# Kernel tuning notes

Measured on AMD Instinct MI355X. Metric: run time of the kernel, lower is better.

Reference implementation:

```python
import jax, jax.numpy as jnp
import numpy as np

B, S, D = 4, 2048, 2048
E = 64           # num_experts
TOPK = 2         # num_experts_per_token


def setup_inputs() -> dict:
    key = jax.random.key(0)
    k1, k2, k3 = jax.random.split(key, 3)
    x_real = jax.random.normal(k1, (B, S, D), dtype=jnp.float32)
    x_imag = jax.random.normal(k2, (B, S, D), dtype=jnp.float32)
    # flax Dense: kernel [in_features, out_features] with lecun_normal-ish scale
    W = jax.random.normal(k3, (2 * D, E), dtype=jnp.float32) / np.sqrt(2.0 * D)
    b = jnp.zeros((E,), dtype=jnp.float32)
    return {"x_real": x_real, "x_imag": x_imag, "W": W, "b": b}


def reference(x_real, x_imag, W, b):
    # amp = |x|, phase = angle(x) for x = x_real + i*x_imag
    amp = jnp.hypot(x_real, x_imag)                 # [B,S,D]
    phase = jnp.arctan2(x_imag, x_real)             # [B,S,D]
    routing_input = jnp.concatenate([amp, phase], axis=-1)  # [B,S,2D]
    scores = jnp.einsum('bsf,fe->bse', routing_input, W) + b  # [B,S,E]
    probs = jax.nn.softmax(scores, axis=-1)
    top_k_probs, top_k_indices = jax.lax.top_k(probs, TOPK)   # [B,S,K]
    top_k_probs = top_k_probs / jnp.sum(top_k_probs, axis=-1, keepdims=True)
    return (top_k_probs, top_k_indices)
```

## Files before the change

### kernel.cpp

```cpp
#include <hip/hip_runtime.h>
#include <math.h>

#define NTOK 8192
#define DD   2048
#define EE   64
#define TSTRIP 16
#define NCH 16
#define PROB_N (NTOK*2)
#define AROW 136
#define F_PSTRIDE (128*4*64*8)

typedef _Float16 f16x8 __attribute__((ext_vector_type(8)));
typedef _Float16 f16x4 __attribute__((ext_vector_type(4)));
typedef float    f32x4 __attribute__((ext_vector_type(4)));

__device__ __forceinline__ f16x8 gload_f16x8(const _Float16* p) {
    f16x8 r;
    asm volatile("global_load_dwordx4 %0, %1, off" : "=v"(r) : "v"(p));
    return r;
}
__device__ __forceinline__ f32x4 gload_f32x4(const float* p) {
    f32x4 r;
    asm volatile("global_load_dwordx4 %0, %1, off" : "=v"(r) : "v"(p));
    return r;
}
#define VMWAIT(n) do { \
    asm volatile("s_waitcnt vmcnt(" #n ")" ::: "memory"); \
    __builtin_amdgcn_sched_barrier(0); \
} while (0)
#define LBAR() do { \
    asm volatile("s_waitcnt lgkmcnt(0)" ::: "memory"); \
    __builtin_amdgcn_s_barrier(); \
    __builtin_amdgcn_sched_barrier(0); \
} while (0)

__device__ __forceinline__ float fast_atan2f(float y, float x) {
    const float ax = __builtin_fabsf(x), ay = __builtin_fabsf(y);
    const float hi = fmaxf(ax, ay), lo = fminf(ax, ay);
    const bool  big = lo > 0.4142135679721832f * hi;
    const float num = big ? (lo - hi) : lo;
    const float den = big ? (lo + hi) : hi;
    float rc = __builtin_amdgcn_rcpf(den);
    rc = rc * fmaf(-den, rc, 2.0f);
    const float z  = num * rc;
    const float z2 = z * z;
    float p = fmaf(z2, 8.05374449538e-2f, -1.38776856032e-1f);
    p = fmaf(z2, p, 1.99777106478e-1f);
    p = fmaf(z2, p, -3.33329491539e-1f);
    float r = fmaf(z * z2, p, z);
    r = r + (big ? 0.78539816339744830962f : 0.0f);
    r = (ay > ax) ? (1.57079632679489661923f - r) : r;
    r = (x < 0.0f) ? (3.14159265358979323846f - r) : r;
    return copysignf(r, y);
}

__device__ __forceinline__ void fsplit2(float x, _Float16& h1, _Float16& h2s) {
    const _Float16 a = (_Float16)x;
    h1 = a;
    h2s = (_Float16)((x - (float)a) * 2048.0f);
}

__global__ __launch_bounds__(256) void wsplit(const float* __restrict__ W,
                                              _Float16* __restrict__ F) {
    const int g  = blockIdx.x * 256 + threadIdx.x;
    const int e  = g & 63;
    const int q  = g >> 6;
    const int d0 = q * 4;
    const int nt = e >> 4;
    const int lane = ((d0 & 31) >> 3) * 16 + (e & 15);
    const int j0 = d0 & 7;
    const int cka = 2 * (d0 >> 5);

    f16x4 a1, a2, p1, p2;
    #pragma unroll
    for (int i = 0; i < 4; ++i) {
        _Float16 h, l;
        fsplit2(W[(size_t)(d0 + i) * EE + e], h, l);      a1[i] = h; a2[i] = l;
        fsplit2(W[(size_t)(DD + d0 + i) * EE + e], h, l); p1[i] = h; p2[i] = l;
    }
    *(f16x4*)&F[((size_t)(0 * 128 + cka)     * 4 + nt) * 512 + lane * 8 + j0] = a1;
    *(f16x4*)&F[((size_t)(1 * 128 + cka)     * 4 + nt) * 512 + lane * 8 + j0] = a2;
    *(f16x4*)&F[((size_t)(0 * 128 + cka + 1) * 4 + nt) * 512 + lane * 8 + j0] = p1;
    *(f16x4*)&F[((size_t)(1 * 128 + cka + 1) * 4 + nt) * 512 + lane * 8 + j0] = p2;
}

__global__ __launch_bounds__(512, 4) void gemm_topk(
    const float* __restrict__ xr, const float* __restrict__ xi,
    const _Float16* __restrict__ F, const float* __restrict__ bias,
    float* __restrict__ out)
{
    __shared__ __align__(16) _Float16 A[2][2][2][TSTRIP][AROW];
    __shared__ float scoreH[2][TSTRIP][EE];

    const int tid = threadIdx.x;
    const int t0  = blockIdx.x * TSTRIP;
    const int wv = tid >> 6, lane = tid & 63;
    const int nt = wv & 3, kh = wv >> 2;
    const int fm = lane & 15, fq = lane >> 4;
    const int kh_s  = tid >> 8;
    const int tok_s = (tid >> 4) & 15;
    const int f4    = tid & 15;

    const float bv = bias[lane];

    const float* prx = xr + (size_t)(t0 + tok_s) * DD + kh_s * 1024 + f4 * 4;
    const float* pix = xi + (size_t)(t0 + tok_s) * DD + kh_s * 1024 + f4 * 4;
    const int posa = 64 * (f4 >> 3) + (f4 & 7) * 4;

    auto sprocess = [&](f32x4 vr, f32x4 vi, int buf) {
        f16x4 a1, a2, p1, p2;
        #pragma unroll
        for (int i = 0; i < 4; ++i) {
            const float amp = __builtin_amdgcn_sqrtf(fmaf(vr[i], vr[i], vi[i] * vi[i]));
            const float ph  = fast_atan2f(vi[i], vr[i]);
            _Float16 h, l;
            fsplit2(amp, h, l); a1[i] = h; a2[i] = l;
            fsplit2(ph,  h, l); p1[i] = h; p2[i] = l;
        }
        *(f16x4*)&A[buf][kh_s][0][tok_s][posa]      = a1;
        *(f16x4*)&A[buf][kh_s][1][tok_s][posa]      = a2;
        *(f16x4*)&A[buf][kh_s][0][tok_s][posa + 32] = p1;
        *(f16x4*)&A[buf][kh_s][1][tok_s][posa + 32] = p2;
    };

    f32x4 accH = (f32x4){0.f, 0.f, 0.f, 0.f};
    f32x4 accL = (f32x4){0.f, 0.f, 0.f, 0.f};

    const _Float16* bbase = F + ((size_t)(kh * 64) * 4 + nt) * 512 + lane * 8;

    f16x8 bh[2][4], bl[2][4];
    f32x4 xrb[2], xib[2];

    xrb[0] = gload_f32x4(prx);
    xib[0] = gload_f32x4(pix);
    #pragma unroll
    for (int j = 0; j < 4; ++j) {
        bh[0][j] = gload_f16x8(bbase + j * 2048);
        bl[0][j] = gload_f16x8(bbase + F_PSTRIDE + j * 2048);
    }
    VMWAIT(8);
    sprocess(xrb[0], xib[0], 0);
    xrb[1] = gload_f32x4(prx + 64);
    xib[1] = gload_f32x4(pix + 64);
    #pragma unroll
    for (int j = 0; j < 4; ++j) {
        bh[1][j] = gload_f16x8(bbase + 8192 + j * 2048);
        bl[1][j] = gload_f16x8(bbase + 8192 + F_PSTRIDE + j * 2048);
    }
    LBAR();

    #pragma unroll
    for (int c = 0; c < NCH; ++c) {
        const int buf = c & 1;
        if (c < NCH - 1) { VMWAIT(10); } else { VMWAIT(0); }
        #pragma unroll
        for (int j = 0; j < 4; ++j) {
            const f16x8 a1 = *(const f16x8*)&A[buf][kh][0][fm][j * 32 + fq * 8];
            const f16x8 a2 = *(const f16x8*)&A[buf][kh][1][fm][j * 32 + fq * 8];
            accH = __builtin_amdgcn_mfma_f32_16x16x32_f16(a1, bh[buf][j], accH, 0, 0, 0);
            accL = __builtin_amdgcn_mfma_f32_16x16x32_f16(a1, bl[buf][j], accL, 0, 0, 0);
            accL = __builtin_amdgcn_mfma_f32_16x16x32_f16(a2, bh[buf][j], accL, 0, 0, 0);
        }
        if (c < NCH - 1) {
            VMWAIT(8);
            sprocess(xrb[buf ^ 1], xib[buf ^ 1], buf ^ 1);
            if (c < NCH - 2) {
                xrb[buf] = gload_f32x4(prx + (c + 2) * 64);
                xib[buf] = gload_f32x4(pix + (c + 2) * 64);
                const _Float16* nb = bbase + (size_t)(c + 2) * 8192;
                #pragma unroll
                for (int j = 0; j < 4; ++j) {
                    bh[buf][j] = gload_f16x8(nb + j * 2048);
                    bl[buf][j] = gload_f16x8(nb + F_PSTRIDE + j * 2048);
                }
            }
            LBAR();
        }
    }

    #pragma unroll
    for (int r = 0; r < 4; ++r)
        scoreH[kh][fq * 4 + r][nt * 16 + fm] = fmaf(accL[r], 4.8828125e-4f, accH[r]);
    __syncthreads();

    #pragma unroll
    for (int rep = 0; rep < 2; ++rep) {
        const int tok = wv * 2 + rep;
        float v1 = scoreH[0][tok][lane] + scoreH[1][tok][lane] + bv;
        float v2 = -INFINITY;
        int   i1 = lane, i2 = 64;
        #pragma unroll
        for (int off = 1; off < 64; off <<= 1) {
            const float ov1 = __shfl_xor(v1, off, 64);
            const int   oi1 = __shfl_xor(i1, off, 64);
            const float ov2 = __shfl_xor(v2, off, 64);
            const int   oi2 = __shfl_xor(i2, off, 64);
            const bool b1 = (ov1 > v1) || (ov1 == v1 && oi1 < i1);
            const float n1 = b1 ? ov1 : v1;  const int ni1 = b1 ? oi1 : i1;
            const float c1 = b1 ? v1  : ov1; const int ci1 = b1 ? i1  : oi1;
            const float c2 = b1 ? ov2 : v2;  const int ci2 = b1 ? oi2 : i2;
            const bool b2 = (c1 > c2) || (c1 == c2 && ci1 < ci2);
            v1 = n1; i1 = ni1;
            v2 = b2 ? c1 : c2; i2 = b2 ? ci1 : ci2;
        }
        if (lane == 0) {
            const int t = t0 + tok;
            const float z  = expf(v2 - v1);
            const float p1 = 1.0f / (1.0f + z);
            const float p2 = z / (1.0f + z);
            out[(size_t)t * 2 + 0] = p1;
            out[(size_t)t * 2 + 1] = p2;
            out[PROB_N + (size_t)t * 2 + 0] = (float)i1;
            out[PROB_N + (size_t)t * 2 + 1] = (float)i2;
        }
    }
}

extern "C" void kernel_launch(void* const* d_in, const int* in_sizes, int n_in,
                              void* d_out, int out_size, void* d_ws, size_t ws_size,
                              hipStream_t stream) {
    const float* xr = (const float*)d_in[0];
    const float* xi = (const float*)d_in[1];
    const float* W  = (const float*)d_in[2];
    const float* b  = (const float*)d_in[3];
    float* out = (float*)d_out;
    _Float16* F = (_Float16*)d_ws;

    wsplit<<<128, 256, 0, stream>>>(W, F);
    gemm_topk<<<NTOK / TSTRIP, 512, 0, stream>>>(xr, xi, F, b, out);
}
```

Baseline: 172.5 us.

## Warp-specialize gemm_topk into producer and MFMA waves with LDS flag handshakes

Splits each 768-thread block into 8 MFMA consumer waves and 4 producer waves. The producers load x and compute amp and phase into a 3-slot LDS ring, and the two sides sync through per-chunk ready and done counters instead of block barriers. The token strip doubles to 32 so each consumer wave issues two MFMA row tiles per B fragment, which halves how often B is loaded from global memory per token. The aim is to overlap the heavy atan2 work with the matrix math. The cost is spin-wait polling, fewer blocks, and more LDS per block.

```diff
diff --git a/kernel.cpp b/kernel.cpp
--- a/kernel.cpp
+++ b/kernel.cpp
@@ -4,8 +4,9 @@
 #define NTOK 8192
 #define DD   2048
 #define EE   64
-#define TSTRIP 16
+#define TSTRIP 32
 #define NCH 16
+#define NSLOT 3
 #define PROB_N (NTOK*2)
 #define AROW 136
 #define F_PSTRIDE (128*4*64*8)
@@ -84,134 +85,174 @@
     *(f16x4*)&F[((size_t)(1 * 128 + cka + 1) * 4 + nt) * 512 + lane * 8 + j0] = p2;
 }
 
-__global__ __launch_bounds__(512, 4) void gemm_topk(
+__global__ __launch_bounds__(768, 3) void gemm_topk(
     const float* __restrict__ xr, const float* __restrict__ xi,
     const _Float16* __restrict__ F, const float* __restrict__ bias,
     float* __restrict__ out)
 {
-    __shared__ __align__(16) _Float16 A[2][2][2][TSTRIP][AROW];
+    __shared__ __align__(16) _Float16 A[NSLOT][2][2][TSTRIP][AROW];
     __shared__ float scoreH[2][TSTRIP][EE];
+    __shared__ int rdy[NCH];
+    __shared__ int dne[NCH];
 
     const int tid = threadIdx.x;
     const int t0  = blockIdx.x * TSTRIP;
     const int wv = tid >> 6, lane = tid & 63;
-    const int nt = wv & 3, kh = wv >> 2;
-    const int fm = lane & 15, fq = lane >> 4;
-    const int kh_s  = tid >> 8;
-    const int tok_s = (tid >> 4) & 15;
-    const int f4    = tid & 15;
-
-    const float bv = bias[lane];
-
-    const float* prx = xr + (size_t)(t0 + tok_s) * DD + kh_s * 1024 + f4 * 4;
-    const float* pix = xi + (size_t)(t0 + tok_s) * DD + kh_s * 1024 + f4 * 4;
-    const int posa = 64 * (f4 >> 3) + (f4 & 7) * 4;
-
-    auto sprocess = [&](f32x4 vr, f32x4 vi, int buf) {
-        f16x4 a1, a2, p1, p2;
-        #pragma unroll
-        for (int i = 0; i < 4; ++i) {
-            const float amp = __builtin_amdgcn_sqrtf(fmaf(vr[i], vr[i], vi[i] * vi[i]));
-            const float ph  = fast_atan2f(vi[i], vr[i]);
-            _Float16 h, l;
-            fsplit2(amp, h, l); a1[i] = h; a2[i] = l;
-            fsplit2(ph,  h, l); p1[i] = h; p2[i] = l;
-        }
-        *(f16x4*)&A[buf][kh_s][0][tok_s][posa]      = a1;
-        *(f16x4*)&A[buf][kh_s][1][tok_s][posa]      = a2;
-        *(f16x4*)&A[buf][kh_s][0][tok_s][posa + 32] = p1;
-        *(f16x4*)&A[buf][kh_s][1][tok_s][posa + 32] = p2;
-    };
-
-    f32x4 accH = (f32x4){0.f, 0.f, 0.f, 0.f};
-    f32x4 accL = (f32x4){0.f, 0.f, 0.f, 0.f};
-
-    const _Float16* bbase = F + ((size_t)(kh * 64) * 4 + nt) * 512 + lane * 8;
-
-    f16x8 bh[2][4], bl[2][4];
-    f32x4 xrb[2], xib[2];
-
-    xrb[0] = gload_f32x4(prx);
-    xib[0] = gload_f32x4(pix);
-    #pragma unroll
-    for (int j = 0; j < 4; ++j) {
-        bh[0][j] = gload_f16x8(bbase + j * 2048);
-        bl[0][j] = gload_f16x8(bbase + F_PSTRIDE + j * 2048);
-    }
-    VMWAIT(8);
-    sprocess(xrb[0], xib[0], 0);
-    xrb[1] = gload_f32x4(prx + 64);
-    xib[1] = gload_f32x4(pix + 64);
-    #pragma unroll
-    for (int j = 0; j < 4; ++j) {
-        bh[1][j] = gload_f16x8(bbase + 8192 + j * 2048);
-        bl[1][j] = gload_f16x8(bbase + 8192 + F_PSTRIDE + j * 2048);
-    }
-    LBAR();
-
-    #pragma unroll
-    for (int c = 0; c < NCH; ++c) {
-        const int buf = c & 1;
-        if (c < NCH - 1) { VMWAIT(10); } else { VMWAIT(0); }
+
+    if (tid < NCH) { rdy[tid] = 0; dne[tid] = 0; }
+
+    if (wv < 8) {
+        const int nt = wv & 3, kh = wv >> 2;
+        const int fm = lane & 15, fq = lane >> 4;
+        const _Float16* bbase = F + ((size_t)(kh * 64) * 4 + nt) * 512 + lane * 8;
+
+        f16x8 bh[2][4], bl[2][4];
         #pragma unroll
         for (int j = 0; j < 4; ++j) {
-            const f16x8 a1 = *(const f16x8*)&A[buf][kh][0][fm][j * 32 + fq * 8];
-            const f16x8 a2 = *(const f16x8*)&A[buf][kh][1][fm][j * 32 + fq * 8];
-            accH = __builtin_amdgcn_mfma_f32_16x16x32_f16(a1, bh[buf][j], accH, 0, 0, 0);
-            accL = __builtin_amdgcn_mfma_f32_16x16x32_f16(a1, bl[buf][j], accL, 0, 0, 0);
-            accL = __builtin_amdgcn_mfma_f32_16x16x32_f16(a2, bh[buf][j], accL, 0, 0, 0);
-        }
-        if (c < NCH - 1) {
-            VMWAIT(8);
-            sprocess(xrb[buf ^ 1], xib[buf ^ 1], buf ^ 1);
-            if (c < NCH - 2) {
-                xrb[buf] = gload_f32x4(prx + (c + 2) * 64);
-                xib[buf] = gload_f32x4(pix + (c + 2) * 64);
-                const _Float16* nb = bbase + (size_t)(c + 2) * 8192;
+            bh[0][j] = gload_f16x8(bbase + j * 2048);
+            bl[0][j] = gload_f16x8(bbase + F_PSTRIDE + j * 2048);
+        }
+        LBAR();
+
+        f32x4 accH0 = (f32x4){0.f,0.f,0.f,0.f}, accL0 = (f32x4){0.f,0.f,0.f,0.f};
+        f32x4 accH1 = (f32x4){0.f,0.f,0.f,0.f}, accL1 = (f32x4){0.f,0.f,0.f,0.f};
+
+        #pragma unroll
+        for (int c = 0; c < NCH; ++c) {
+            const int buf = c & 1;
+            if (c < NCH - 1) {
+                const _Float16* nb = bbase + (size_t)(c + 1) * 8192;
                 #pragma unroll
                 for (int j = 0; j < 4; ++j) {
-                    bh[buf][j] = gload_f16x8(nb + j * 2048);
-                    bl[buf][j] = gload_f16x8(nb + F_PSTRIDE + j * 2048);
+                    bh[buf ^ 1][j] = gload_f16x8(nb + j * 2048);
+                    bl[buf ^ 1][j] = gload_f16x8(nb + F_PSTRIDE + j * 2048);
                 }
             }
-            LBAR();
-        }
+            while (*(volatile int*)&rdy[c] < 4) __builtin_amdgcn_s_sleep(1);
+            __builtin_amdgcn_sched_barrier(0);
+            if (c < NCH - 1) { VMWAIT(8); } else { VMWAIT(0); }
+            #pragma unroll
+            for (int j = 0; j < 4; ++j) {
+                const int co = j * 32 + fq * 8;
+                const f16x8 a10 = *(const f16x8*)&A[c % NSLOT][kh][0][fm][co];
+                const f16x8 a20 = *(const f16x8*)&A[c % NSLOT][kh][1][fm][co];
+                const f16x8 a11 = *(const f16x8*)&A[c % NSLOT][kh][0][fm + 16][co];
+                const f16x8 a21 = *(const f16x8*)&A[c % NSLOT][kh][1][fm + 16][co];
+                accH0 = __builtin_amdgcn_mfma_f32_16x16x32_f16(a10, bh[buf][j], accH0, 0, 0, 0);
+                accL0 = __builtin_amdgcn_mfma_f32_16x16x32_f16(a10, bl[buf][j], accL0, 0, 0, 0);
+                accL0 = __builtin_amdgcn_mfma_f32_16x16x32_f16(a20, bh[buf][j], accL0, 0, 0, 0);
+                accH1 = __builtin_amdgcn_mfma_f32_16x16x32_f16(a11, bh[buf][j], accH1, 0, 0, 0);
+                accL1 = __builtin_amdgcn_mfma_f32_16x16x32_f16(a11, bl[buf][j], accL1, 0, 0, 0);
+                accL1 = __builtin_amdgcn_mfma_f32_16x16x32_f16(a21, bh[buf][j], accL1, 0, 0, 0);
+            }
+            asm volatile("s_waitcnt lgkmcnt(0)" ::: "memory");
+            if (lane == 0) atomicAdd(&dne[c], 1);
+        }
+        #pragma unroll
+        for (int r = 0; r < 4; ++r) {
+            scoreH[kh][fq * 4 + r][nt * 16 + fm]      = fmaf(accL0[r], 4.8828125e-4f, accH0[r]);
+            scoreH[kh][16 + fq * 4 + r][nt * 16 + fm] = fmaf(accL1[r], 4.8828125e-4f, accH1[r]);
+        }
+    } else {
+        const int ptid = tid - 512;
+        const int f8   = ptid & 7;
+        const int tokp = ptid >> 3;
+        const float* prx = xr + (size_t)(t0 + tokp) * DD + f8 * 8;
+        const float* pix = xi + (size_t)(t0 + tokp) * DD + f8 * 8;
+        const int wpos = (f8 >> 2) * 64 + (f8 & 3) * 8;
+
+        f32x4 R0[4], I0[4], R1[4], I1[4];
+
+        auto pload = [&](int c, f32x4* R, f32x4* I) {
+            #pragma unroll
+            for (int k2 = 0; k2 < 2; ++k2)
+                #pragma unroll
+                for (int h = 0; h < 2; ++h) {
+                    R[k2 * 2 + h] = gload_f32x4(prx + k2 * 1024 + c * 64 + h * 4);
+                    I[k2 * 2 + h] = gload_f32x4(pix + k2 * 1024 + c * 64 + h * 4);
+                }
+        };
+        auto pstore = [&](int c, f32x4* R, f32x4* I) {
+            const int slot = c % NSLOT;
+            #pragma unroll
+            for (int k2 = 0; k2 < 2; ++k2) {
+                f16x8 a1, a2, p1, p2;
+                #pragma unroll
+                for (int h = 0; h < 2; ++h)
+                    #pragma unroll
+                    for (int i = 0; i < 4; ++i) {
+                        const float rr = R[k2 * 2 + h][i], im = I[k2 * 2 + h][i];
+                        const float amp = __builtin_amdgcn_sqrtf(fmaf(rr, rr, im * im));
+                        const float ph  = fast_atan2f(im, rr);
+                        _Float16 hh, ll;
+                        fsplit2(amp, hh, ll); a1[h * 4 + i] = hh; a2[h * 4 + i] = ll;
+                        fsplit2(ph,  hh, ll); p1[h * 4 + i] = hh; p2[h * 4 + i] = ll;
+                    }
+                *(f16x8*)&A[slot][k2][0][tokp][wpos]      = a1;
+                *(f16x8*)&A[slot][k2][1][tokp][wpos]      = a2;
+                *(f16x8*)&A[slot][k2][0][tokp][wpos + 32] = p1;
+                *(f16x8*)&A[slot][k2][1][tokp][wpos + 32] = p2;
+            }
+        };
+
+        pload(0, R0, I0);
+        pload(1, R1, I1);
+        LBAR();
+
+        #define PBODY(c, R, I, DO_ISSUE, WN) do { \
+            if ((c) >= 3) { while (*(volatile int*)&dne[(c) - 3] < 8) __builtin_amdgcn_s_sleep(1); } \
+            __builtin_amdgcn_sched_barrier(0); \
+            VMWAIT(WN); \
+            pstore((c), R, I); \
+            asm volatile("s_waitcnt lgkmcnt(0)" ::: "memory"); \
+            if (lane == 0) atomicAdd(&rdy[(c)], 1); \
+            if (DO_ISSUE) pload((c) + 2, R, I); \
+        } while (0)
+
+        for (int cc = 0; cc < 7; ++cc) {
+            const int c0 = 2 * cc, c1 = 2 * cc + 1;
+            PBODY(c0, R0, I0, 1, 8);
+            PBODY(c1, R1, I1, 1, 8);
+        }
+        PBODY(14, R0, I0, 0, 8);
+        PBODY(15, R1, I1, 0, 0);
+        #undef PBODY
     }
 
-    #pragma unroll
-    for (int r = 0; r < 4; ++r)
-        scoreH[kh][fq * 4 + r][nt * 16 + fm] = fmaf(accL[r], 4.8828125e-4f, accH[r]);
-    __syncthreads();
-
-    #pragma unroll
-    for (int rep = 0; rep < 2; ++rep) {
-        const int tok = wv * 2 + rep;
-        float v1 = scoreH[0][tok][lane] + scoreH[1][tok][lane] + bv;
-        float v2 = -INFINITY;
-        int   i1 = lane, i2 = 64;
-        #pragma unroll
-        for (int off = 1; off < 64; off <<= 1) {
-            const float ov1 = __shfl_xor(v1, off, 64);
-            const int   oi1 = __shfl_xor(i1, off, 64);
-            const float ov2 = __shfl_xor(v2, off, 64);
-            const int   oi2 = __shfl_xor(i2, off, 64);
-            const bool b1 = (ov1 > v1) || (ov1 == v1 && oi1 < i1);
-            const float n1 = b1 ? ov1 : v1;  const int ni1 = b1 ? oi1 : i1;
-            const float c1 = b1 ? v1  : ov1; const int ci1 = b1 ? i1  : oi1;
-            const float c2 = b1 ? ov2 : v2;  const int ci2 = b1 ? oi2 : i2;
-            const bool b2 = (c1 > c2) || (c1 == c2 && ci1 < ci2);
-            v1 = n1; i1 = ni1;
-            v2 = b2 ? c1 : c2; i2 = b2 ? ci1 : ci2;
-        }
-        if (lane == 0) {
-            const int t = t0 + tok;
-            const float z  = expf(v2 - v1);
-            const float p1 = 1.0f / (1.0f + z);
-            const float p2 = z / (1.0f + z);
-            out[(size_t)t * 2 + 0] = p1;
-            out[(size_t)t * 2 + 1] = p2;
-            out[PROB_N + (size_t)t * 2 + 0] = (float)i1;
-            out[PROB_N + (size_t)t * 2 + 1] = (float)i2;
+    LBAR();
+
+    if (wv < 8) {
+        const float bv = bias[lane];
+        #pragma unroll
+        for (int rep = 0; rep < 4; ++rep) {
+            const int tok = wv * 4 + rep;
+            float v1 = scoreH[0][tok][lane] + scoreH[1][tok][lane] + bv;
+            float v2 = -INFINITY;
+            int   i1 = lane, i2 = 64;
+            #pragma unroll
+            for (int off = 1; off < 64; off <<= 1) {
+                const float ov1 = __shfl_xor(v1, off, 64);
+                const int   oi1 = __shfl_xor(i1, off, 64);
+                const float ov2 = __shfl_xor(v2, off, 64);
+                const int   oi2 = __shfl_xor(i2, off, 64);
+                const bool b1 = (ov1 > v1) || (ov1 == v1 && oi1 < i1);
+                const float n1 = b1 ? ov1 : v1;  const int ni1 = b1 ? oi1 : i1;
+                const float c1 = b1 ? v1  : ov1; const int ci1 = b1 ? i1  : oi1;
+                const float c2 = b1 ? ov2 : v2;  const int ci2 = b1 ? oi2 : i2;
+                const bool b2 = (c1 > c2) || (c1 == c2 && ci1 < ci2);
+                v1 = n1; i1 = ni1;
+                v2 = b2 ? c1 : c2; i2 = b2 ? ci1 : ci2;
+            }
+            if (lane == 0) {
+                const int t = t0 + tok;
+                const float z  = expf(v2 - v1);
+                const float p1 = 1.0f / (1.0f + z);
+                const float p2 = z / (1.0f + z);
+                out[(size_t)t * 2 + 0] = p1;
+                out[(size_t)t * 2 + 1] = p2;
+                out[PROB_N + (size_t)t * 2 + 0] = (float)i1;
+                out[PROB_N + (size_t)t * 2 + 1] = (float)i2;
+            }
         }
     }
 }
@@ -227,5 +268,5 @@
     _Float16* F = (_Float16*)d_ws;
 
     wsplit<<<128, 256, 0, stream>>>(W, F);
-    gemm_topk<<<NTOK / TSTRIP, 512, 0, stream>>>(xr, xi, F, b, out);
-}
+    gemm_topk<<<NTOK / TSTRIP, 768, 0, stream>>>(xr, xi, F, b, out);
+}
```

New measurement: 170.1 us. About the same (-1.4%).
